# Kernel tuning notes

Measured on AMD Instinct MI355X. Metric: run time of the kernel, lower is better.

Reference implementation:

```python
import jax, jax.numpy as jnp
import numpy as np

B, N, W, C = 32, 2048, 64, 1024  # batch, memory_size, word_size, controller_size
EPS = 1e-8


def setup_inputs() -> dict:
    key = jax.random.key(0)
    ks = jax.random.split(key, 10)
    s = 0.02
    return {
        "controller_output": jax.random.normal(ks[0], (B, C), jnp.float32),
        "prev_read_weights": jax.random.uniform(ks[1], (B, N), jnp.float32),
        "prev_write_weight": jax.random.uniform(ks[2], (B, N), jnp.float32),
        "memory": jax.random.normal(ks[3], (B, N, W), jnp.float32),
        "usage": jax.random.uniform(ks[4], (B, N), jnp.float32),
        "Wk": (jax.random.normal(ks[5], (W, C), jnp.float32) * s), "bk": jnp.zeros((W,), jnp.float32),
        "Wb": (jax.random.normal(ks[6], (1, C), jnp.float32) * s), "bb": jnp.zeros((1,), jnp.float32),
        "Ws": (jax.random.normal(ks[7], (3, C), jnp.float32) * s), "bs": jnp.zeros((3,), jnp.float32),
        "Wg": (jax.random.normal(ks[8], (1, C), jnp.float32) * s), "bg": jnp.zeros((1,), jnp.float32),
    }


def reference(controller_output, prev_read_weights, prev_write_weight, memory, usage,
              Wk, bk, Wb, bb, Ws, bs, Wg, bg):
    # --- content addressing ---
    k = jnp.tanh(controller_output @ Wk.T + bk)                     # [B, W]
    beta = jax.nn.softplus(controller_output @ Wb.T + bb)[:, 0]     # [B]
    sim = jnp.einsum('bnw,bw->bn', memory, k)                       # [B, N]
    content_weights = jax.nn.softmax(sim * beta[:, None], axis=-1)  # [B, N]

    # --- shift-matrix directional addressing ---
    shift = jax.nn.softmax(controller_output @ Ws.T + bs, axis=-1)  # [B, 3]
    sc = (-shift[:, 0] + shift[:, 2])[:, None, None]                # [B, 1, 1]
    idx = jnp.arange(N, dtype=jnp.float32)
    dist = (idx[:, None] - idx[None, :] + N / 2) % N                # [N, N]
    kernel = jnp.exp(-(dist[None] ** 2) / (2.0 * sc ** 2 + EPS))    # [B, N, N]
    kernel = kernel / (kernel.sum(axis=2, keepdims=True) + EPS)
    directional_weights = jnp.einsum('bn,bnm->bm', prev_read_weights, kernel)  # [B, N]

    # --- allocation: sort usage, cumprod of (1-usage), scatter back ---
    order = jnp.argsort(usage, axis=-1)                             # [B, N]
    sorted_usage = jnp.take_along_axis(usage, order, axis=-1)
    cumprod = jnp.cumprod(1.0 - sorted_usage, axis=-1)
    brow = jnp.arange(usage.shape[0])[:, None]
    allocation_weights = jnp.zeros_like(usage).at[brow, order].set(cumprod)

    # --- combine ---
    write_gate = jax.nn.sigmoid(controller_output @ Wg.T + bg)[:, 0]  # [B]
    write_weights = write_gate[:, None] * (
        0.5 * content_weights + 0.5 * directional_weights * allocation_weights)
    return (write_weights, content_weights, directional_weights, allocation_weights)
```

## Files before the change

### kernel.cpp

```cpp
#include <hip/hip_runtime.h>

#define BB 32
#define NN 2048
#define WW 64
#define CC 1024
#define NTAP 17
#define NB 512
#define EPSF 1e-8f
#define TOKEN 0x5A5A5A5Au

#define WS_Q  0
#define WS_P  (BB*NN)
#define WS_G  (BB*NN + BB*4)
#define WS_FA (BB*NN + BB*5)
#define WS_FS (BB*NN + BB*6)

__global__ __launch_bounds__(1024) void k_one(
    const float* __restrict__ co, const float* __restrict__ rdw,
    const float* __restrict__ usage, const float* __restrict__ mem,
    const float* __restrict__ Wk, const float* __restrict__ bk,
    const float* __restrict__ Wb, const float* __restrict__ bb,
    const float* __restrict__ Ws, const float* __restrict__ bs,
    const float* __restrict__ Wg, const float* __restrict__ bg,
    float* __restrict__ ws, float* __restrict__ out)
{
    __shared__ float co_s[CC];
    __shared__ __align__(16) float k_s[WW + 4];
    __shared__ float r_s[NN];
    __shared__ unsigned long long skey[NN];
    __shared__ float slog[NN];
    __shared__ float alloc_s[NN];
    __shared__ unsigned hist[NB];
    __shared__ float binlog[NB];
    __shared__ unsigned binStart[NB];
    __shared__ unsigned cursor[NB];
    __shared__ float binpre[NB];
    __shared__ unsigned uw[8];
    __shared__ float fw[8];
    __shared__ float dot4[16][4];
    __shared__ float sred[16];
    __shared__ float scalars[8];
    __shared__ float wd_s[NTAP];
    __shared__ float bcast[2];

    const int tid = threadIdx.x, wave = tid >> 6, lane = tid & 63;
    const int bid = blockIdx.x;
    unsigned* flagA = (unsigned*)(ws + WS_FA);
    unsigned* flagS = (unsigned*)(ws + WS_FS);

    if (bid < BB) {
        const int b = bid;
        if (tid < NB) { hist[tid] = 0u; binlog[tid] = 0.f; }
        co_s[tid] = co[(size_t)b * CC + tid];
        r_s[tid]        = rdw[(size_t)b * NN + tid];
        r_s[tid + 1024] = rdw[(size_t)b * NN + tid + 1024];
        float u0 = usage[(size_t)b * NN + tid];
        float u1 = usage[(size_t)b * NN + tid + 1024];
        __syncthreads();
        float lg0 = __logf(1.0f - u0), lg1 = __logf(1.0f - u1);
        int bin0 = (int)(u0 * NB); bin0 = bin0 < 0 ? 0 : (bin0 > NB - 1 ? NB - 1 : bin0);
        int bin1 = (int)(u1 * NB); bin1 = bin1 < 0 ? 0 : (bin1 > NB - 1 ? NB - 1 : bin1);
        atomicAdd(&hist[bin0], 1u); atomicAdd(&binlog[bin0], lg0);
        atomicAdd(&hist[bin1], 1u); atomicAdd(&binlog[bin1], lg1);
        {
            float cv = co_s[tid];
            float p0 = cv * Ws[tid], p1 = cv * Ws[CC + tid],
                  p2 = cv * Ws[2 * CC + tid], p3 = cv * Wg[tid];
            #pragma unroll
            for (int off = 32; off; off >>= 1) {
                p0 += __shfl_xor(p0, off); p1 += __shfl_xor(p1, off);
                p2 += __shfl_xor(p2, off); p3 += __shfl_xor(p3, off);
            }
            if (lane == 0) {
                dot4[wave][0] = p0; dot4[wave][1] = p1;
                dot4[wave][2] = p2; dot4[wave][3] = p3;
            }
        }
        __syncthreads();
        unsigned hv = 0u; float bv = 0.f, fi = 0.f; unsigned ui = 0u;
        if (tid < NB) {
            hv = hist[tid]; bv = binlog[tid];
            ui = hv; fi = bv;
            #pragma unroll
            for (int off = 1; off < 64; off <<= 1) {
                unsigned tu = __shfl_up(ui, off);
                float    tf = __shfl_up(fi, off);
                if (lane >= off) { ui += tu; fi += tf; }
            }
            if (lane == 63) { uw[wave] = ui; fw[wave] = fi; }
        }
        if (tid < 4) {
            float s = 0.f;
            #pragma unroll
            for (int w = 0; w < 16; w++) s += dot4[w][tid];
            scalars[tid] = s + ((tid < 3) ? bs[tid] : bg[0]);
        }
        __syncthreads();
        if (tid < 8) {
            unsigned v = uw[tid]; float f = fw[tid];
            #pragma unroll
            for (int off = 1; off < 8; off <<= 1) {
                unsigned tu = __shfl_up(v, off);
                float    tf = __shfl_up(f, off);
                if (tid >= off) { v += tu; f += tf; }
            }
            uw[tid] = v; fw[tid] = f;
        } else if (tid == 16) {
            float g = scalars[3];
            float gate = 1.f / (1.f + __expf(-g));
            scalars[6] = gate;
            __hip_atomic_store(ws + WS_G + b, gate,
                               __ATOMIC_RELAXED, __HIP_MEMORY_SCOPE_AGENT);
            float s0 = scalars[0], s1 = scalars[1], s2 = scalars[2];
            float m = fmaxf(s0, fmaxf(s1, s2));
            float e0 = __expf(s0 - m), e1 = __expf(s1 - m), e2 = __expf(s2 - m);
            float inv = 1.f / (e0 + e1 + e2);
            float sc = (e2 - e0) * inv;
            float den = 2.f * sc * sc + EPSF;
            float w[NTAP]; float S = 0.f;
            #pragma unroll
            for (int d = 0; d < NTAP; d++) { w[d] = __expf(-(float)(d * d) / den); S += w[d]; }
            float invS = 1.f / (S + EPSF);
            #pragma unroll
            for (int d = 0; d < NTAP; d++) wd_s[d] = w[d] * invS;
        }
        __syncthreads();
        if (tid < NB) {
            unsigned woff = wave ? uw[wave - 1] : 0u;
            float    foff = wave ? fw[wave - 1] : 0.f;
            unsigned st = woff + ui - hv;
            binStart[tid] = st; cursor[tid] = st;
            binpre[tid] = foff + fi - bv;
        }
        __syncthreads();
        unsigned long long key0 = ((unsigned long long)__float_as_uint(u0) << 32) | (unsigned)tid;
        unsigned long long key1 = ((unsigned long long)__float_as_uint(u1) << 32) | (unsigned)(tid + 1024);
        {
            unsigned p0 = atomicAdd(&cursor[bin0], 1u);
            skey[p0] = key0; slog[p0] = lg0;
            unsigned p1 = atomicAdd(&cursor[bin1], 1u);
            skey[p1] = key1; slog[p1] = lg1;
        }
        __syncthreads();
        float* aout = out + 3 * (size_t)BB * NN + (size_t)b * NN;
        #pragma unroll
        for (int pp = 0; pp < 2; pp++) {
            int p = tid + pp * 1024;
            unsigned long long kp = skey[p];
            float up = __uint_as_float((unsigned)(kp >> 32));
            int c = (int)(up * NB); c = c < 0 ? 0 : (c > NB - 1 ? NB - 1 : c);
            unsigned st = binStart[c], cnt = hist[c];
            float s = binpre[c];
            for (unsigned q = 0; q < cnt; q++)
                s += (skey[st + q] <= kp) ? slog[st + q] : 0.f;
            float a = __expf(s);
            unsigned oidx = (unsigned)(kp & 0xFFFFFFFFu);
            alloc_s[oidx] = a;
            aout[oidx] = a;
        }
        __syncthreads();
        const float gate = scalars[6];
        float dw0 = 0.f, dw1 = 0.f;
        #pragma unroll
        for (int d = 0; d < NTAP; d++) {
            float w = wd_s[d];
            dw0 = fmaf(w, r_s[(tid + 1024 + d) & (NN - 1)], dw0);
            dw1 = fmaf(w, r_s[(tid + d) & (NN - 1)], dw1);
        }
        out[2 * (size_t)BB * NN + (size_t)b * NN + tid]        = dw0;
        out[2 * (size_t)BB * NN + (size_t)b * NN + tid + 1024] = dw1;
        ws[WS_Q + (size_t)b * NN + tid]        = 0.5f * gate * dw0 * alloc_s[tid];
        ws[WS_Q + (size_t)b * NN + tid + 1024] = 0.5f * gate * dw1 * alloc_s[tid + 1024];
        __syncthreads();
        if (tid == 0) {
            __threadfence();
            __hip_atomic_store(&flagA[b], TOKEN,
                               __ATOMIC_RELEASE, __HIP_MEMORY_SCOPE_AGENT);
        }
    } else {
        const int i = bid - BB;
        const int b = i >> 2, j = i & 3;
        const int base = j * 512;
        co_s[tid] = co[(size_t)b * CC + tid];
        __syncthreads();
        const float4* co4 = reinterpret_cast<const float4*>(co_s);
        #pragma unroll
        for (int rr = 0; rr < 4; ++rr) {
            const int o = wave + rr * 16;
            const float4* wrow = reinterpret_cast<const float4*>(Wk + (size_t)o * CC);
            float s = 0.f;
            #pragma unroll
            for (int ch = 0; ch < 4; ++ch) {
                float4 wv = wrow[ch * 64 + lane];
                float4 cv = co4[ch * 64 + lane];
                s += wv.x * cv.x + wv.y * cv.y + wv.z * cv.z + wv.w * cv.w;
            }
            #pragma unroll
            for (int off = 32; off; off >>= 1) s += __shfl_xor(s, off);
            if (lane == 0) k_s[o] = tanhf(s + bk[o]);
        }
        if (wave == 0) {
            const float4* wrow = reinterpret_cast<const float4*>(Wb);
            float s = 0.f;
            #pragma unroll
            for (int ch = 0; ch < 4; ++ch) {
                float4 wv = wrow[ch * 64 + lane];
                float4 cv = co4[ch * 64 + lane];
                s += wv.x * cv.x + wv.y * cv.y + wv.z * cv.z + wv.w * cv.w;
            }
            #pragma unroll
            for (int off = 32; off; off >>= 1) s += __shfl_xor(s, off);
            if (lane == 0) k_s[WW] = s + bb[0];
        }
        __syncthreads();
        const float xb = k_s[WW];
        const float beta = (xb > 20.f) ? xb : log1pf(__expf(xb));
        const int lane16 = tid & 15, group = tid >> 4;
        const float4 k4 = reinterpret_cast<const float4*>(k_s)[lane16];
        float4 mr[8];
        #pragma unroll
        for (int it = 0; it < 8; ++it) {
            const int row = base + it * 64 + group;
            mr[it] = *reinterpret_cast<const float4*>(
                mem + ((size_t)b * NN + row) * WW + lane16 * 4);
        }
        float esum = 0.f;
        #pragma unroll
        for (int it = 0; it < 8; ++it) {
            float s = mr[it].x * k4.x + mr[it].y * k4.y
                    + mr[it].z * k4.z + mr[it].w * k4.w;
            s += __shfl_xor(s, 1); s += __shfl_xor(s, 2);
            s += __shfl_xor(s, 4); s += __shfl_xor(s, 8);
            if (lane16 == 0) {
                float e = __expf(s * beta);
                slog[it * 64 + group] = e;
                esum += e;
            }
        }
        #pragma unroll
        for (int off = 32; off; off >>= 1) esum += __shfl_xor(esum, off);
        if (lane == 0) sred[wave] = esum;
        __syncthreads();
        if (tid == 0) {
            float v = 0.f;
            #pragma unroll
            for (int w = 0; w < 16; w++) v += sred[w];
            __hip_atomic_store(ws + WS_P + (size_t)b * 4 + j, v,
                               __ATOMIC_RELAXED, __HIP_MEMORY_SCOPE_AGENT);
            __hip_atomic_store(&flagS[b * 4 + j], TOKEN,
                               __ATOMIC_RELEASE, __HIP_MEMORY_SCOPE_AGENT);
        }
        if (tid < 3) {
            const int s = (j + 1 + tid) & 3;
            while (__hip_atomic_load(&flagS[b * 4 + s],
                                     __ATOMIC_ACQUIRE, __HIP_MEMORY_SCOPE_AGENT) != TOKEN)
                __builtin_amdgcn_s_sleep(8);
        } else if (tid == 3) {
            while (__hip_atomic_load(&flagA[b],
                                     __ATOMIC_ACQUIRE, __HIP_MEMORY_SCOPE_AGENT) != TOKEN)
                __builtin_amdgcn_s_sleep(8);
        }
        __syncthreads();
        if (tid == 0) {
            float D = 0.f;
            #pragma unroll
            for (int s = 0; s < 4; ++s)
                D += __hip_atomic_load(ws + WS_P + (size_t)b * 4 + s,
                                       __ATOMIC_RELAXED, __HIP_MEMORY_SCOPE_AGENT);
            bcast[0] = 1.f / D;
            bcast[1] = __hip_atomic_load(ws + WS_G + b,
                                         __ATOMIC_RELAXED, __HIP_MEMORY_SCOPE_AGENT);
        }
        __syncthreads();
        const float invD = bcast[0], gate = bcast[1];
        if (tid < 512) {
            const int n = base + tid;
            const float qv = __hip_atomic_load(ws + WS_Q + (size_t)b * NN + n,
                                               __ATOMIC_RELAXED, __HIP_MEMORY_SCOPE_AGENT);
            const float c = slog[tid] * invD;
            out[(size_t)BB * NN + (size_t)b * NN + n] = c;
            out[(size_t)b * NN + n] = fmaf(0.5f * gate, c, qv);
        }
    }
}

extern "C" void kernel_launch(void* const* d_in, const int* in_sizes, int n_in,
                              void* d_out, int out_size, void* d_ws, size_t ws_size,
                              hipStream_t stream) {
    const float* co    = (const float*)d_in[0];
    const float* rdw   = (const float*)d_in[1];
    const float* mem   = (const float*)d_in[3];
    const float* usage = (const float*)d_in[4];
    const float* Wk    = (const float*)d_in[5];
    const float* bk    = (const float*)d_in[6];
    const float* Wb    = (const float*)d_in[7];
    const float* bb    = (const float*)d_in[8];
    const float* Ws_   = (const float*)d_in[9];
    const float* bs    = (const float*)d_in[10];
    const float* Wg    = (const float*)d_in[11];
    const float* bg    = (const float*)d_in[12];
    float* out = (float*)d_out;
    float* wsf = (float*)d_ws;

    hipLaunchKernelGGL(k_one, dim3(BB + 128), dim3(1024), 0, stream,
                       co, rdw, usage, mem, Wk, bk, Wb, bb, Ws_, bs, Wg, bg,
                       wsf, out);
}
```

Measured before the change: 20.90 us.

## Move final combine into per-batch blocks and drop reverse flag wait

The content-similarity blocks now write their unnormalized exponentials to workspace and publish a partial sum, then exit without waiting. The per-batch allocation blocks wait on the four partial-sum flags and do the normalization and final write-weight combine themselves, which removes the allocation-to-content flag and the intermediate Q buffer. The memory row loads are also issued before the key projection so their latency overlaps the matvec. The cost is extra global traffic for the exponentials, and the per-batch block now stalls until the content blocks finish. Only the content blocks publish flags and the per-batch block consumes them, so cross-block dependencies no longer run both ways.

```diff
diff --git a/kernel.cpp b/kernel.cpp
--- a/kernel.cpp
+++ b/kernel.cpp
@@ -9,11 +9,9 @@
 #define EPSF 1e-8f
 #define TOKEN 0x5A5A5A5Au
 
-#define WS_Q  0
+#define WS_X  0
 #define WS_P  (BB*NN)
-#define WS_G  (BB*NN + BB*4)
-#define WS_FA (BB*NN + BB*5)
-#define WS_FS (BB*NN + BB*6)
+#define WS_FS (BB*NN + BB*4)
 
 __global__ __launch_bounds__(1024) void k_one(
     const float* __restrict__ co, const float* __restrict__ rdw,
@@ -41,11 +39,10 @@
     __shared__ float sred[16];
     __shared__ float scalars[8];
     __shared__ float wd_s[NTAP];
-    __shared__ float bcast[2];
+    __shared__ float bcast[1];
 
     const int tid = threadIdx.x, wave = tid >> 6, lane = tid & 63;
     const int bid = blockIdx.x;
-    unsigned* flagA = (unsigned*)(ws + WS_FA);
     unsigned* flagS = (unsigned*)(ws + WS_FS);
 
     if (bid < BB) {
@@ -107,10 +104,7 @@
             uw[tid] = v; fw[tid] = f;
         } else if (tid == 16) {
             float g = scalars[3];
-            float gate = 1.f / (1.f + __expf(-g));
-            scalars[6] = gate;
-            __hip_atomic_store(ws + WS_G + b, gate,
-                               __ATOMIC_RELAXED, __HIP_MEMORY_SCOPE_AGENT);
+            scalars[6] = 1.f / (1.f + __expf(-g));
             float s0 = scalars[0], s1 = scalars[1], s2 = scalars[2];
             float m = fmaxf(s0, fmaxf(s1, s2));
             float e0 = __expf(s0 - m), e1 = __expf(s1 - m), e2 = __expf(s2 - m);
@@ -169,18 +163,41 @@
         }
         out[2 * (size_t)BB * NN + (size_t)b * NN + tid]        = dw0;
         out[2 * (size_t)BB * NN + (size_t)b * NN + tid + 1024] = dw1;
-        ws[WS_Q + (size_t)b * NN + tid]        = 0.5f * gate * dw0 * alloc_s[tid];
-        ws[WS_Q + (size_t)b * NN + tid + 1024] = 0.5f * gate * dw1 * alloc_s[tid + 1024];
-        __syncthreads();
-        if (tid == 0) {
-            __threadfence();
-            __hip_atomic_store(&flagA[b], TOKEN,
-                               __ATOMIC_RELEASE, __HIP_MEMORY_SCOPE_AGENT);
-        }
+
+        if (tid < 4) {
+            while (__hip_atomic_load(&flagS[b * 4 + tid],
+                                     __ATOMIC_RELAXED, __HIP_MEMORY_SCOPE_AGENT) != TOKEN)
+                __builtin_amdgcn_s_sleep(8);
+        }
+        __syncthreads();
+        if (tid == 0) __threadfence();
+        __syncthreads();
+        const float* P = ws + WS_P + (size_t)b * 4;
+        const float D = P[0] + P[1] + P[2] + P[3];
+        if (tid == 0) bcast[0] = 1.f / D;
+        __syncthreads();
+        const float invD = bcast[0];
+        const float e0 = ws[WS_X + (size_t)b * NN + tid];
+        const float e1 = ws[WS_X + (size_t)b * NN + tid + 1024];
+        const float c0 = e0 * invD, c1 = e1 * invD;
+        out[(size_t)BB * NN + (size_t)b * NN + tid]        = c0;
+        out[(size_t)BB * NN + (size_t)b * NN + tid + 1024] = c1;
+        out[(size_t)b * NN + tid] =
+            gate * fmaf(0.5f, c0, 0.5f * dw0 * alloc_s[tid]);
+        out[(size_t)b * NN + tid + 1024] =
+            gate * fmaf(0.5f, c1, 0.5f * dw1 * alloc_s[tid + 1024]);
     } else {
         const int i = bid - BB;
         const int b = i >> 2, j = i & 3;
         const int base = j * 512;
+        const int lane16 = tid & 15, group = tid >> 4;
+        float4 mr[8];
+        #pragma unroll
+        for (int it = 0; it < 8; ++it) {
+            const int row = base + it * 64 + group;
+            mr[it] = *reinterpret_cast<const float4*>(
+                mem + ((size_t)b * NN + row) * WW + lane16 * 4);
+        }
         co_s[tid] = co[(size_t)b * CC + tid];
         __syncthreads();
         const float4* co4 = reinterpret_cast<const float4*>(co_s);
@@ -215,25 +232,19 @@
         __syncthreads();
         const float xb = k_s[WW];
         const float beta = (xb > 20.f) ? xb : log1pf(__expf(xb));
-        const int lane16 = tid & 15, group = tid >> 4;
         const float4 k4 = reinterpret_cast<const float4*>(k_s)[lane16];
-        float4 mr[8];
+        float esum = 0.f;
         #pragma unroll
         for (int it = 0; it < 8; ++it) {
             const int row = base + it * 64 + group;
-            mr[it] = *reinterpret_cast<const float4*>(
-                mem + ((size_t)b * NN + row) * WW + lane16 * 4);
-        }
-        float esum = 0.f;
-        #pragma unroll
-        for (int it = 0; it < 8; ++it) {
             float s = mr[it].x * k4.x + mr[it].y * k4.y
                     + mr[it].z * k4.z + mr[it].w * k4.w;
             s += __shfl_xor(s, 1); s += __shfl_xor(s, 2);
             s += __shfl_xor(s, 4); s += __shfl_xor(s, 8);
             if (lane16 == 0) {
                 float e = __expf(s * beta);
-                slog[it * 64 + group] = e;
+                __hip_atomic_store(ws + WS_X + (size_t)b * NN + row, e,
+                                   __ATOMIC_RELAXED, __HIP_MEMORY_SCOPE_AGENT);
                 esum += e;
             }
         }
@@ -249,37 +260,6 @@
                                __ATOMIC_RELAXED, __HIP_MEMORY_SCOPE_AGENT);
             __hip_atomic_store(&flagS[b * 4 + j], TOKEN,
                                __ATOMIC_RELEASE, __HIP_MEMORY_SCOPE_AGENT);
-        }
-        if (tid < 3) {
-            const int s = (j + 1 + tid) & 3;
-            while (__hip_atomic_load(&flagS[b * 4 + s],
-                                     __ATOMIC_ACQUIRE, __HIP_MEMORY_SCOPE_AGENT) != TOKEN)
-                __builtin_amdgcn_s_sleep(8);
-        } else if (tid == 3) {
-            while (__hip_atomic_load(&flagA[b],
-                                     __ATOMIC_ACQUIRE, __HIP_MEMORY_SCOPE_AGENT) != TOKEN)
-                __builtin_amdgcn_s_sleep(8);
-        }
-        __syncthreads();
-        if (tid == 0) {
-            float D = 0.f;
-            #pragma unroll
-            for (int s = 0; s < 4; ++s)
-                D += __hip_atomic_load(ws + WS_P + (size_t)b * 4 + s,
-                                       __ATOMIC_RELAXED, __HIP_MEMORY_SCOPE_AGENT);
-            bcast[0] = 1.f / D;
-            bcast[1] = __hip_atomic_load(ws + WS_G + b,
-                                         __ATOMIC_RELAXED, __HIP_MEMORY_SCOPE_AGENT);
-        }
-        __syncthreads();
-        const float invD = bcast[0], gate = bcast[1];
-        if (tid < 512) {
-            const int n = base + tid;
-            const float qv = __hip_atomic_load(ws + WS_Q + (size_t)b * NN + n,
-                                               __ATOMIC_RELAXED, __HIP_MEMORY_SCOPE_AGENT);
-            const float c = slog[tid] * invD;
-            out[(size_t)BB * NN + (size_t)b * NN + n] = c;
-            out[(size_t)b * NN + n] = fmaf(0.5f * gate, c, qv);
         }
     }
 }
```

Result: faster. 19.67 us (-5.9%).
